# Kernel tuning notes

Hardware: AMD Instinct MI355X
Metric: run time of the kernel (lower is better)

The kernel has to match this reference:

```python
import jax, jax.numpy as jnp
import numpy as np

NUM_EXPERTS = 8


def setup_inputs() -> dict:
    key = jax.random.key(0)
    k1, k2, k3, k4, k5 = jax.random.split(key, 5)
    T, D, DFF, E, K = 2048, 2048, 1024, NUM_EXPERTS, 2
    hidden_states = jax.random.normal(k1, (T, D), dtype=jnp.float32)
    w1 = jax.random.normal(k2, (E, 2 * DFF, D), dtype=jnp.float32) * 0.02
    w2 = jax.random.normal(k3, (E, D, DFF), dtype=jnp.float32) * 0.02
    topk_weights = jax.random.uniform(k4, (T, K), dtype=jnp.float32)
    topk_weights = topk_weights / jnp.sum(topk_weights, axis=-1, keepdims=True)
    topk_ids = jax.random.randint(k5, (T, K), 0, E, dtype=jnp.int32)
    return {"hidden_states": hidden_states, "w1": w1, "w2": w2,
            "topk_weights": topk_weights, "topk_ids": topk_ids}


def _expert_fn(x, w1_e, w2_e):
    # x: [T, D], w1_e: [2*DFF, D], w2_e: [D, DFF]
    gu = x @ w1_e.T                      # [T, 2*DFF]
    dff = w2_e.shape[1]
    gate, up = gu[:, :dff], gu[:, dff:]
    h = jax.nn.silu(gate) * up           # SiLU-and-mul activation
    return h @ w2_e.T                    # [T, D]


def reference(hidden_states, w1, w2, topk_weights, topk_ids):
    T = hidden_states.shape[0]
    E = w1.shape[0]
    # route[t, e] = sum_k topk_weights[t,k] * (topk_ids[t,k] == e)
    route = jnp.zeros((T, E), dtype=hidden_states.dtype)
    route = route.at[jnp.arange(T)[:, None], topk_ids].add(topk_weights)
    # per-expert dense GEMMs (E is small and fixed), then weighted combine
    outs = jax.vmap(lambda w1_e, w2_e: _expert_fn(hidden_states, w1_e, w2_e))(w1, w2)  # [E, T, D]
    return jnp.einsum('te,etd->td', route, outs)
```

## Files before the change

### kernel.cpp

```cpp
#include <hip/hip_runtime.h>
#include <hip/hip_bf16.h>
#include <stdint.h>

typedef __attribute__((ext_vector_type(4))) float f32x4;
typedef __attribute__((ext_vector_type(8))) short bf16x8;
typedef unsigned short u16;

#define T_TOK   2048
#define D_DIM   2048
#define DFF_DIM 1024
#define NEXP    8
#define TOPK    2
#define NROWS   (T_TOK * TOPK)
#define BM      128
#define BK      64
#define MAX_MB  40

__device__ __forceinline__ u16 f2bf(float f) {
    union { float f; uint32_t u; } v; v.f = f;
    return (u16)((v.u + 0x7FFFu + ((v.u >> 16) & 1u)) >> 16);
}

__device__ __forceinline__ void gll16(const u16* gsrc, const u16* lds) {
    __builtin_amdgcn_global_load_lds(
        (const __attribute__((address_space(1))) uint32_t*)gsrc,
        (__attribute__((address_space(3))) uint32_t*)lds, 16, 0, 0);
}

__device__ __forceinline__ bf16x8 lds_read8_lin(const u16* base, int row, int inner) {
    return *(const bf16x8*)((const char*)base + row * 128 + inner);
}
__device__ __forceinline__ bf16x8 lds_read8_swz(const u16* base, int row, int inner) {
    int off = row * 128 + (inner ^ ((row & 7) << 4));
    return *(const bf16x8*)((const char*)base + off);
}

__global__ void cvt_x_kernel(const float* __restrict__ X, u16* __restrict__ Xb) {
    int idx = (blockIdx.x * 256 + threadIdx.x) * 8;
    f32x4 a = *(const f32x4*)(X + idx);
    f32x4 b = *(const f32x4*)(X + idx + 4);
    bf16x8 v;
#pragma unroll
    for (int j = 0; j < 4; ++j) { v[j] = (short)f2bf(a[j]); v[j + 4] = (short)f2bf(b[j]); }
    *(bf16x8*)(Xb + idx) = v;
}

__global__ void route_kernel(const int* __restrict__ topk_ids,
                             const float* __restrict__ topk_w,
                             int* __restrict__ sched,
                             int* __restrict__ row_token,
                             float* __restrict__ row_w) {
    __shared__ int cnt[NEXP], off[NEXP], cur[NEXP];
    const int tid = threadIdx.x;
    if (tid < NEXP) cnt[tid] = 0;
    __syncthreads();
    for (int p = tid; p < NROWS; p += blockDim.x)
        atomicAdd(&cnt[topk_ids[p]], 1);
    __syncthreads();
    if (tid == 0) {
        int acc = 0, mb = 0;
        for (int e = 0; e < NEXP; ++e) {
            off[e] = acc;
            int c = cnt[e];
            for (int m0 = 0; m0 < c; m0 += BM) {
                sched[1 + 3 * mb] = e;
                sched[2 + 3 * mb] = acc + m0;
                sched[3 + 3 * mb] = (c - m0 < BM) ? (c - m0) : BM;
                ++mb;
            }
            acc += c;
        }
        sched[0] = mb;
    }
    if (tid < NEXP) cur[tid] = 0;
    __syncthreads();
    for (int p = tid; p < NROWS; p += blockDim.x) {
        int e = topk_ids[p];
        int slot = off[e] + atomicAdd(&cur[e], 1);
        row_token[slot] = p / TOPK;
        row_w[slot]     = topk_w[p];
    }
}

__global__ __launch_bounds__(256, 3)
void gemm1_kernel(const u16* __restrict__ Xb, const float* __restrict__ w1,
                  const int* __restrict__ sched, const int* __restrict__ row_token,
                  u16* __restrict__ H) {
    __shared__ u16 lA[2][BM * BK];
    __shared__ u16 lB[BM * BK];

    const int mb = blockIdx.y;
    if (mb >= sched[0]) return;
    const int e    = sched[1 + 3 * mb];
    const int m0   = sched[2 + 3 * mb];
    const int mlen = sched[3 + 3 * mb];
    const int n0   = blockIdx.x * 64;

    const int tid  = threadIdx.x;
    const int lane = tid & 63;
    const int wave = tid >> 6;
    const int wm = wave >> 1, wn = wave & 1;
    const int lr = lane & 15, lk = lane >> 4;

    const u16* asrc[4];
    int aoff[4];
#pragma unroll
    for (int i = 0; i < 4; ++i) {
        int R = i * 32 + wave * 8 + (lane >> 3);
        int grow = m0 + R; if (grow > NROWS - 1) grow = NROWS - 1;
        int tok = row_token[grow];
        asrc[i] = Xb + (size_t)tok * D_DIM + (lane & 7) * 8;
        aoff[i] = i * 2048 + wave * 512;
    }
    const float* bptr[4];
    int wroff[4];
#pragma unroll
    for (int i = 0; i < 4; ++i) {
        int chunk = i * 256 + tid;
        int row = chunk >> 3, c8 = chunk & 7;
        int gcol = (row < 64) ? (n0 + row) : (DFF_DIM + n0 + (row - 64));
        bptr[i] = w1 + ((size_t)e * (2 * DFF_DIM) + gcol) * D_DIM + c8 * 8;
        wroff[i] = row * 128 + ((c8 * 16) ^ ((row & 7) << 4));
    }

    f32x4 rb[4][2];
    f32x4 accg[4][2], accu[4][2];
#pragma unroll
    for (int m = 0; m < 4; ++m)
#pragma unroll
        for (int n = 0; n < 2; ++n) {
            accg[m][n] = (f32x4){0.f, 0.f, 0.f, 0.f};
            accu[m][n] = (f32x4){0.f, 0.f, 0.f, 0.f};
        }

#pragma unroll
    for (int i = 0; i < 4; ++i) gll16(asrc[i], &lA[0][aoff[i]]);
#pragma unroll
    for (int i = 0; i < 4; ++i) {
        rb[i][0] = *(const f32x4*)(bptr[i]);
        rb[i][1] = *(const f32x4*)(bptr[i] + 4);
    }
#pragma unroll
    for (int i = 0; i < 4; ++i) {
        bf16x8 vb;
#pragma unroll
        for (int j = 0; j < 4; ++j) { vb[j] = (short)f2bf(rb[i][0][j]); vb[j + 4] = (short)f2bf(rb[i][1][j]); }
        *(bf16x8*)((char*)lB + wroff[i]) = vb;
    }
    __syncthreads();

    int cur = 0;
    const int KT = D_DIM / BK;
    for (int kt = 0; kt < KT; ++kt) {
        if (kt + 1 < KT) {
            int k0 = (kt + 1) * BK;
#pragma unroll
            for (int i = 0; i < 4; ++i) gll16(asrc[i] + k0, &lA[cur ^ 1][aoff[i]]);
#pragma unroll
            for (int i = 0; i < 4; ++i) {
                rb[i][0] = *(const f32x4*)(bptr[i] + k0);
                rb[i][1] = *(const f32x4*)(bptr[i] + k0 + 4);
            }
        }
        asm volatile("" ::: "memory");
#pragma unroll
        for (int ks = 0; ks < 2; ++ks) {
            const int inner = ks * 64 + lk * 16;
            bf16x8 af[4], bg[2], bu[2];
#pragma unroll
            for (int m = 0; m < 4; ++m)
                af[m] = lds_read8_lin(lA[cur], wm * 64 + m * 16 + lr, inner);
#pragma unroll
            for (int n = 0; n < 2; ++n) {
                bg[n] = lds_read8_swz(lB, wn * 32 + n * 16 + lr, inner);
                bu[n] = lds_read8_swz(lB, 64 + wn * 32 + n * 16 + lr, inner);
            }
#pragma unroll
            for (int m = 0; m < 4; ++m)
#pragma unroll
                for (int n = 0; n < 2; ++n) {
                    accg[m][n] = __builtin_amdgcn_mfma_f32_16x16x32_bf16(af[m], bg[n], accg[m][n], 0, 0, 0);
                    accu[m][n] = __builtin_amdgcn_mfma_f32_16x16x32_bf16(af[m], bu[n], accu[m][n], 0, 0, 0);
                }
        }
        __syncthreads();
        if (kt + 1 < KT) {
#pragma unroll
            for (int i = 0; i < 4; ++i) {
                bf16x8 vb;
#pragma unroll
                for (int j = 0; j < 4; ++j) { vb[j] = (short)f2bf(rb[i][0][j]); vb[j + 4] = (short)f2bf(rb[i][1][j]); }
                *(bf16x8*)((char*)lB + wroff[i]) = vb;
            }
        }
        __syncthreads();
        cur ^= 1;
    }

#pragma unroll
    for (int m = 0; m < 4; ++m)
#pragma unroll
        for (int n = 0; n < 2; ++n)
#pragma unroll
            for (int r = 0; r < 4; ++r) {
                int rloc = wm * 64 + m * 16 + (lane >> 4) * 4 + r;
                if (rloc < mlen) {
                    int col = wn * 32 + n * 16 + lr;
                    float g = accg[m][n][r], u = accu[m][n][r];
                    float h = (g / (1.f + __expf(-g))) * u;
                    H[(size_t)(m0 + rloc) * DFF_DIM + n0 + col] = f2bf(h);
                }
            }
}

__global__ __launch_bounds__(256, 3)
void gemm2_kernel(const u16* __restrict__ H, const float* __restrict__ w2,
                  const int* __restrict__ sched, const int* __restrict__ row_token,
                  const float* __restrict__ row_w, float* __restrict__ out) {
    __shared__ u16 lA[2][BM * BK];
    __shared__ u16 lB[BM * BK];

    const int mb = blockIdx.y;
    if (mb >= sched[0]) return;
    const int e    = sched[1 + 3 * mb];
    const int m0   = sched[2 + 3 * mb];
    const int mlen = sched[3 + 3 * mb];
    const int n0   = blockIdx.x * 128;

    const int tid  = threadIdx.x;
    const int lane = tid & 63;
    const int wave = tid >> 6;
    const int wm = wave >> 1, wn = wave & 1;
    const int lr = lane & 15, lk = lane >> 4;

    const u16* asrc[4];
    int aoff[4];
#pragma unroll
    for (int i = 0; i < 4; ++i) {
        int R = i * 32 + wave * 8 + (lane >> 3);
        int grow = m0 + R; if (grow > NROWS - 1) grow = NROWS - 1;
        asrc[i] = H + (size_t)grow * DFF_DIM + (lane & 7) * 8;
        aoff[i] = i * 2048 + wave * 512;
    }
    const float* bptr[4];
    int wroff[4];
#pragma unroll
    for (int i = 0; i < 4; ++i) {
        int chunk = i * 256 + tid;
        int row = chunk >> 3, c8 = chunk & 7;
        bptr[i] = w2 + ((size_t)e * D_DIM + (n0 + row)) * DFF_DIM + c8 * 8;
        wroff[i] = row * 128 + ((c8 * 16) ^ ((row & 7) << 4));
    }

    f32x4 rb[4][2];
    f32x4 acc[4][4];
#pragma unroll
    for (int m = 0; m < 4; ++m)
#pragma unroll
        for (int n = 0; n < 4; ++n) acc[m][n] = (f32x4){0.f, 0.f, 0.f, 0.f};

#pragma unroll
    for (int i = 0; i < 4; ++i) gll16(asrc[i], &lA[0][aoff[i]]);
#pragma unroll
    for (int i = 0; i < 4; ++i) {
        rb[i][0] = *(const f32x4*)(bptr[i]);
        rb[i][1] = *(const f32x4*)(bptr[i] + 4);
    }
#pragma unroll
    for (int i = 0; i < 4; ++i) {
        bf16x8 vb;
#pragma unroll
        for (int j = 0; j < 4; ++j) { vb[j] = (short)f2bf(rb[i][0][j]); vb[j + 4] = (short)f2bf(rb[i][1][j]); }
        *(bf16x8*)((char*)lB + wroff[i]) = vb;
    }
    __syncthreads();

    int cur = 0;
    const int KT = DFF_DIM / BK;
    for (int kt = 0; kt < KT; ++kt) {
        if (kt + 1 < KT) {
            int k0 = (kt + 1) * BK;
#pragma unroll
            for (int i = 0; i < 4; ++i) gll16(asrc[i] + k0, &lA[cur ^ 1][aoff[i]]);
#pragma unroll
            for (int i = 0; i < 4; ++i) {
                rb[i][0] = *(const f32x4*)(bptr[i] + k0);
                rb[i][1] = *(const f32x4*)(bptr[i] + k0 + 4);
            }
        }
        asm volatile("" ::: "memory");
#pragma unroll
        for (int ks = 0; ks < 2; ++ks) {
            const int inner = ks * 64 + lk * 16;
            bf16x8 af[4], bfr[4];
#pragma unroll
            for (int m = 0; m < 4; ++m)
                af[m] = lds_read8_lin(lA[cur], wm * 64 + m * 16 + lr, inner);
#pragma unroll
            for (int n = 0; n < 4; ++n)
                bfr[n] = lds_read8_swz(lB, wn * 64 + n * 16 + lr, inner);
#pragma unroll
            for (int m = 0; m < 4; ++m)
#pragma unroll
                for (int n = 0; n < 4; ++n)
                    acc[m][n] = __builtin_amdgcn_mfma_f32_16x16x32_bf16(af[m], bfr[n], acc[m][n], 0, 0, 0);
        }
        __syncthreads();
        if (kt + 1 < KT) {
#pragma unroll
            for (int i = 0; i < 4; ++i) {
                bf16x8 vb;
#pragma unroll
                for (int j = 0; j < 4; ++j) { vb[j] = (short)f2bf(rb[i][0][j]); vb[j + 4] = (short)f2bf(rb[i][1][j]); }
                *(bf16x8*)((char*)lB + wroff[i]) = vb;
            }
        }
        __syncthreads();
        cur ^= 1;
    }

#pragma unroll
    for (int m = 0; m < 4; ++m)
#pragma unroll
        for (int n = 0; n < 4; ++n)
#pragma unroll
            for (int r = 0; r < 4; ++r) {
                int rloc = wm * 64 + m * 16 + (lane >> 4) * 4 + r;
                if (rloc < mlen) {
                    int grow = m0 + rloc;
                    int tok  = row_token[grow];
                    float w  = row_w[grow];
                    int col  = wn * 64 + n * 16 + lr;
                    atomicAdd(&out[(size_t)tok * D_DIM + n0 + col], acc[m][n][r] * w);
                }
            }
}

extern "C" void kernel_launch(void* const* d_in, const int* in_sizes, int n_in,
                              void* d_out, int out_size, void* d_ws, size_t ws_size,
                              hipStream_t stream) {
    const float* X  = (const float*)d_in[0];
    const float* w1 = (const float*)d_in[1];
    const float* w2 = (const float*)d_in[2];
    const float* tw = (const float*)d_in[3];
    const int*   ti = (const int*)d_in[4];

    int*   sched     = (int*)d_ws;
    int*   row_token = (int*)((char*)d_ws + 512);
    float* row_w     = (float*)((char*)d_ws + 512 + 4 * NROWS);
    u16*   Xb        = (u16*)((char*)d_ws + 65536);
    u16*   H         = (u16*)((char*)d_ws + 65536 + (size_t)T_TOK * D_DIM * 2);

    route_kernel<<<1, 256, 0, stream>>>(ti, tw, sched, row_token, row_w);
    cvt_x_kernel<<<(T_TOK * D_DIM) / (256 * 8), 256, 0, stream>>>(X, Xb);
    hipMemsetAsync(d_out, 0, (size_t)out_size * sizeof(float), stream);
    gemm1_kernel<<<dim3(DFF_DIM / 64, MAX_MB), 256, 0, stream>>>(Xb, w1, sched, row_token, H);
    gemm2_kernel<<<dim3(D_DIM / 128, MAX_MB), 256, 0, stream>>>(H, w2, sched, row_token, row_w, (float*)d_out);
}
```

Before: 161.7 us.

## Swizzle A-tile LDS layout and remap grid for XCD-aware block scheduling

The activation tile loaded via global_load_lds now has its source columns XOR-permuted by row so it lands in LDS in a swizzled layout. The MFMA operand reads use the swizzled accessor, which is meant to remove LDS bank conflicts on A. Both GEMMs also switch to a 1D grid whose block index is remapped so that consecutive blocks on each XCD share the same expert row-block, aiming for better L2 reuse of weights. The bf16 conversion is replaced with the library intrinsic.

After: 160.6 us. About the same (-0.7%).

```diff
diff --git a/kernel.cpp b/kernel.cpp
--- a/kernel.cpp
+++ b/kernel.cpp
@@ -15,10 +15,13 @@
 #define BM      128
 #define BK      64
 #define MAX_MB  40
+#define NBLK1   16
+#define NBLK2   16
+#define GRID_G  (NBLK1 * MAX_MB)
 
 __device__ __forceinline__ u16 f2bf(float f) {
-    union { float f; uint32_t u; } v; v.f = f;
-    return (u16)((v.u + 0x7FFFu + ((v.u >> 16) & 1u)) >> 16);
+    __hip_bfloat16 h = __float2bfloat16(f);
+    return *reinterpret_cast<u16*>(&h);
 }
 
 __device__ __forceinline__ void gll16(const u16* gsrc, const u16* lds) {
@@ -27,9 +30,6 @@
         (__attribute__((address_space(3))) uint32_t*)lds, 16, 0, 0);
 }
 
-__device__ __forceinline__ bf16x8 lds_read8_lin(const u16* base, int row, int inner) {
-    return *(const bf16x8*)((const char*)base + row * 128 + inner);
-}
 __device__ __forceinline__ bf16x8 lds_read8_swz(const u16* base, int row, int inner) {
     int off = row * 128 + (inner ^ ((row & 7) << 4));
     return *(const bf16x8*)((const char*)base + off);
@@ -89,12 +89,14 @@
     __shared__ u16 lA[2][BM * BK];
     __shared__ u16 lB[BM * BK];
 
-    const int mb = blockIdx.y;
+    const int bid = blockIdx.x;
+    const int swz = (bid & 7) * (GRID_G / 8) + (bid >> 3);
+    const int mb  = swz >> 4;
     if (mb >= sched[0]) return;
     const int e    = sched[1 + 3 * mb];
     const int m0   = sched[2 + 3 * mb];
     const int mlen = sched[3 + 3 * mb];
-    const int n0   = blockIdx.x * 64;
+    const int n0   = (swz & 15) * 64;
 
     const int tid  = threadIdx.x;
     const int lane = tid & 63;
@@ -109,7 +111,7 @@
         int R = i * 32 + wave * 8 + (lane >> 3);
         int grow = m0 + R; if (grow > NROWS - 1) grow = NROWS - 1;
         int tok = row_token[grow];
-        asrc[i] = Xb + (size_t)tok * D_DIM + (lane & 7) * 8;
+        asrc[i] = Xb + (size_t)tok * D_DIM + (size_t)(((lane & 7) ^ (R & 7)) * 8);
         aoff[i] = i * 2048 + wave * 512;
     }
     const float* bptr[4];
@@ -169,7 +171,7 @@
             bf16x8 af[4], bg[2], bu[2];
 #pragma unroll
             for (int m = 0; m < 4; ++m)
-                af[m] = lds_read8_lin(lA[cur], wm * 64 + m * 16 + lr, inner);
+                af[m] = lds_read8_swz(lA[cur], wm * 64 + m * 16 + lr, inner);
 #pragma unroll
             for (int n = 0; n < 2; ++n) {
                 bg[n] = lds_read8_swz(lB, wn * 32 + n * 16 + lr, inner);
@@ -220,12 +222,14 @@
     __shared__ u16 lA[2][BM * BK];
     __shared__ u16 lB[BM * BK];
 
-    const int mb = blockIdx.y;
+    const int bid = blockIdx.x;
+    const int swz = (bid & 7) * (GRID_G / 8) + (bid >> 3);
+    const int mb  = swz >> 4;
     if (mb >= sched[0]) return;
     const int e    = sched[1 + 3 * mb];
     const int m0   = sched[2 + 3 * mb];
     const int mlen = sched[3 + 3 * mb];
-    const int n0   = blockIdx.x * 128;
+    const int n0   = (swz & 15) * 128;
 
     const int tid  = threadIdx.x;
     const int lane = tid & 63;
@@ -239,7 +243,7 @@
     for (int i = 0; i < 4; ++i) {
         int R = i * 32 + wave * 8 + (lane >> 3);
         int grow = m0 + R; if (grow > NROWS - 1) grow = NROWS - 1;
-        asrc[i] = H + (size_t)grow * DFF_DIM + (lane & 7) * 8;
+        asrc[i] = H + (size_t)grow * DFF_DIM + (size_t)(((lane & 7) ^ (R & 7)) * 8);
         aoff[i] = i * 2048 + wave * 512;
     }
     const float* bptr[4];
@@ -295,7 +299,7 @@
             bf16x8 af[4], bfr[4];
 #pragma unroll
             for (int m = 0; m < 4; ++m)
-                af[m] = lds_read8_lin(lA[cur], wm * 64 + m * 16 + lr, inner);
+                af[m] = lds_read8_swz(lA[cur], wm * 64 + m * 16 + lr, inner);
 #pragma unroll
             for (int n = 0; n < 4; ++n)
                 bfr[n] = lds_read8_swz(lB, wn * 64 + n * 16 + lr, inner);
@@ -354,6 +358,6 @@
     route_kernel<<<1, 256, 0, stream>>>(ti, tw, sched, row_token, row_w);
     cvt_x_kernel<<<(T_TOK * D_DIM) / (256 * 8), 256, 0, stream>>>(X, Xb);
     hipMemsetAsync(d_out, 0, (size_t)out_size * sizeof(float), stream);
-    gemm1_kernel<<<dim3(DFF_DIM / 64, MAX_MB), 256, 0, stream>>>(Xb, w1, sched, row_token, H);
-    gemm2_kernel<<<dim3(D_DIM / 128, MAX_MB), 256, 0, stream>>>(H, w2, sched, row_token, row_w, (float*)d_out);
-}
+    gemm1_kernel<<<GRID_G, 256, 0, stream>>>(Xb, w1, sched, row_token, H);
+    gemm2_kernel<<<GRID_G, 256, 0, stream>>>(H, w2, sched, row_token, row_w, (float*)d_out);
+}
```
